# Kernel tuning notes

Hardware: AMD Instinct MI355X
Metric: run time of the kernel (lower is better)

## Reference

```python
import jax, jax.numpy as jnp
import numpy as np

B, N, DIM, EMB_H, EXP, K = 1, 1024, 64, 64, 4, 16


def setup_inputs() -> dict:
    key = jax.random.key(0)
    ks = jax.random.split(key, 12)
    s = lambda k, *shape: jax.random.normal(k, shape, dtype=jnp.float32) * 0.05
    return {
        "x": jax.random.normal(ks[0], (B, N, DIM), dtype=jnp.float32),
        "pos": jax.random.normal(ks[1], (B, N, 3), dtype=jnp.float32),
        "Wq": s(ks[2], DIM, DIM),
        "Wk": s(ks[3], DIM, DIM),
        "Wv": s(ks[4], DIM, DIM),
        "P1": s(ks[5], 3, EMB_H), "pb1": jnp.zeros((EMB_H,), jnp.float32),
        "P2": s(ks[6], EMB_H, DIM), "pb2": jnp.zeros((DIM,), jnp.float32),
        "A1": s(ks[7], DIM, DIM * EXP), "ab1": jnp.zeros((DIM * EXP,), jnp.float32),
        "A2": s(ks[8], DIM * EXP, DIM), "ab2": jnp.zeros((DIM,), jnp.float32),
        "nneighbors": K,
    }


def reference(x, pos, Wq, Wk, Wv, P1, pb1, P2, pb2, A1, ab1, A2, ab2, nneighbors):
    b, n, d = x.shape
    q = x @ Wq            # [b,n,d]
    k = x @ Wk
    v = x @ Wv
    qk_rel = q[:, :, None, :] - k[:, None, :, :]          # [b,n,n,d]
    rel_pos = pos[:, :, None, :] - pos[:, None, :, :]      # [b,n,n,3]
    rel_pos_emb = jax.nn.relu(rel_pos @ P1 + pb1) @ P2 + pb2  # [b,n,n,d]
    # kNN selection on euclidean distance (smallest nneighbors)
    rel_dist = jnp.linalg.norm(rel_pos, axis=-1)           # [b,n,n]
    _, idx = jax.lax.top_k(-rel_dist, nneighbors)          # [b,n,K]
    bidx = jnp.arange(b)[:, None, None]
    v_g = v[bidx, idx]                                     # [b,n,K,d]
    qk_g = jnp.take_along_axis(qk_rel, idx[..., None], axis=2)        # [b,n,K,d]
    rpe_g = jnp.take_along_axis(rel_pos_emb, idx[..., None], axis=2)  # [b,n,K,d]
    v_g = v_g + rpe_g
    sim = jax.nn.relu((qk_g + rpe_g) @ A1 + ab1) @ A2 + ab2  # [b,n,K,d]
    attn = jax.nn.softmax(sim, axis=-2)                      # softmax over neighbors
    agg = jnp.sum(attn * v_g, axis=2)                        # [b,n,d]
    return agg
```

## Files before the change

### kernel.cpp

```cpp
#include <hip/hip_runtime.h>

#define NPTS 1024
#define DIMD 64
#define KNN  16
#define HID  256
#define EMBH 64

typedef short short8 __attribute__((ext_vector_type(8)));
typedef float f32x4  __attribute__((ext_vector_type(4)));

__device__ __forceinline__ short f2bf(float x) {
    unsigned u = __float_as_uint(x);
    unsigned r = (u + 0x7fffu + ((u >> 16) & 1u)) >> 16;
    return (short)r;
}
__device__ __forceinline__ float bf2f(short s) {
    return __uint_as_float(((unsigned)(unsigned short)s) << 16);
}

#define AOFF(k, m) ((((k) >> 3) * 16 + (m)) * 8 + ((k) & 7))

__device__ __host__ __forceinline__ int frag_off(int K, int k, int n) {
    int T = n >> 4, c = k >> 5, q = (k >> 3) & 3, j = k & 7;
    int lane = (q << 4) | (n & 15);
    return ((T * (K >> 5) + c) * 64 + lane) * 8 + j;
}

#define A1HI 0
#define A1LO 16384
#define A2HI 32768
#define A2LO 49152
#define WKHI 65536
#define WKLO 69632
#define WVHI 73728
#define WVLO 77824
#define P2HI 81920
#define P2LO 86016

__global__ __launch_bounds__(256) void prep_weights(
    const float* __restrict__ A1, const float* __restrict__ A2,
    const float* __restrict__ Wk, const float* __restrict__ Wv,
    const float* __restrict__ P2, short* __restrict__ ws)
{
    int e = blockIdx.x * 256 + threadIdx.x;
    float v; int hi_base, lo_base, off;
    if (e < 16384)      { int k = e >> 8, n = e & 255;               v = A1[e];
                          hi_base = A1HI; lo_base = A1LO; off = frag_off(64,  k, n); }
    else if (e < 32768) { int t = e - 16384; int k = t >> 6, n = t & 63; v = A2[t];
                          hi_base = A2HI; lo_base = A2LO; off = frag_off(256, k, n); }
    else if (e < 36864) { int t = e - 32768; int k = t >> 6, n = t & 63; v = Wk[t];
                          hi_base = WKHI; lo_base = WKLO; off = frag_off(64,  k, n); }
    else if (e < 40960) { int t = e - 36864; int k = t >> 6, n = t & 63; v = Wv[t];
                          hi_base = WVHI; lo_base = WVLO; off = frag_off(64,  k, n); }
    else if (e < 45056) { int t = e - 40960; int k = t >> 6, n = t & 63; v = P2[t];
                          hi_base = P2HI; lo_base = P2LO; off = frag_off(64,  k, n); }
    else return;
    short h = f2bf(v);
    short l = f2bf(v - bf2f(h));
    ws[hi_base + off] = h;
    ws[lo_base + off] = l;
}

__global__ __launch_bounds__(256, 4) void ptl_fused(
    const float* __restrict__ x,  const float* __restrict__ pos,
    const float* __restrict__ Wq,
    const float* __restrict__ P1, const float* __restrict__ pb1,
    const float* __restrict__ pb2,
    const float* __restrict__ ab1, const float* __restrict__ ab2,
    const short* __restrict__ ws,
    float* __restrict__ out)
{
    __shared__ __align__(16) short a_xn_hi[16*64],  a_xn_lo[16*64];
    __shared__ __align__(16) short a_es_hi[16*64],  a_es_lo[16*64];
    __shared__ __align__(16) short a_h_hi [16*64],  a_h_lo [16*64];
    __shared__ __align__(16) short a_hd_hi[16*256], a_hd_lo[16*256];
    __shared__ __align__(16) float s_vg[16*68];
    __shared__ __align__(16) float s_sim[16*68];
    __shared__ float s_q[DIMD];
    __shared__ float s_cd[64];
    __shared__ int   s_ci[64];
    __shared__ int   s_idx[KNN];

    const int i    = blockIdx.x;
    const int tid  = threadIdx.x;
    const int lane = tid & 63;
    const int w    = tid >> 6;
    const int q4   = lane >> 4;
    const int col  = lane & 15;

    const float px = pos[i*3+0], py = pos[i*3+1], pz = pos[i*3+2];

    {
        const int base = w * 256;
        float du[4];
        #pragma unroll
        for (int u = 0; u < 4; u++) {
            int j = base + u * 64 + lane;
            float dx = __fsub_rn(px, pos[j*3+0]);
            float dy = __fsub_rn(py, pos[j*3+1]);
            float dz = __fsub_rn(pz, pos[j*3+2]);
            float s  = __fadd_rn(__fadd_rn(__fmul_rn(dx,dx), __fmul_rn(dy,dy)), __fmul_rn(dz,dz));
            du[u] = __fsqrt_rn(s);
        }
        for (int sel = 0; sel < KNN; sel++) {
            float mv = du[0]; int mu = 0;
            #pragma unroll
            for (int u = 1; u < 4; u++) if (du[u] < mv) { mv = du[u]; mu = u; }
            int mj = base + mu * 64 + lane;
            #pragma unroll
            for (int off = 32; off > 0; off >>= 1) {
                float ov = __shfl_xor(mv, off);
                int   oj = __shfl_xor(mj, off);
                if (ov < mv || (ov == mv && oj < mj)) { mv = ov; mj = oj; }
            }
            if (lane == 0) { s_cd[w * 16 + sel] = mv; s_ci[w * 16 + sel] = mj; }
            #pragma unroll
            for (int u = 0; u < 4; u++) if (base + u * 64 + lane == mj) du[u] = 3.0e38f;
        }
    }
    __syncthreads();

    if (w == 0) {
        float md = s_cd[lane]; int mi = s_ci[lane];
        for (int sel = 0; sel < KNN; sel++) {
            float mv = md; int mj = mi;
            #pragma unroll
            for (int off = 32; off > 0; off >>= 1) {
                float ov = __shfl_xor(mv, off);
                int   oj = __shfl_xor(mj, off);
                if (ov < mv || (ov == mv && oj < mj)) { mv = ov; mj = oj; }
            }
            if (lane == 0) s_idx[sel] = mj;
            if (mi == mj) md = 3.0e38f;
        }
    } else if (w == 1) {
        int d = lane;
        const float4* xr = (const float4*)(x + i * DIMD);
        float aq = 0.f;
        #pragma unroll
        for (int cb = 0; cb < DIMD / 4; cb++) {
            float4 xv = xr[cb];
            const float* wq = Wq + (cb*4) * DIMD + d;
            aq = fmaf(xv.x, wq[0*DIMD], aq); aq = fmaf(xv.y, wq[1*DIMD], aq);
            aq = fmaf(xv.z, wq[2*DIMD], aq); aq = fmaf(xv.w, wq[3*DIMD], aq);
        }
        s_q[d] = aq;
    }
    __syncthreads();

    #pragma unroll
    for (int u = 0; u < 4; u++) {
        int t = tid + 256 * u;
        int kk = t >> 6, c = t & 63;
        int j = s_idx[kk];
        int ao = AOFF(c, kk);
        float xv = x[j * DIMD + c];
        short xh = f2bf(xv);
        a_xn_hi[ao] = xh;
        a_xn_lo[ao] = f2bf(xv - bf2f(xh));
        float dx = px - pos[j*3+0];
        float dy = py - pos[j*3+1];
        float dz = pz - pos[j*3+2];
        float a = pb1[c];
        a = fmaf(dx, P1[0*EMBH+c], a);
        a = fmaf(dy, P1[1*EMBH+c], a);
        a = fmaf(dz, P1[2*EMBH+c], a);
        a = fmaxf(a, 0.0f);
        short eh = f2bf(a);
        a_es_hi[ao] = eh;
        a_es_lo[ao] = f2bf(a - bf2f(eh));
    }
    __syncthreads();

    const short8* wsv  = (const short8*)ws;
    const short8* xnh  = (const short8*)a_xn_hi;
    const short8* xnl  = (const short8*)a_xn_lo;
    const short8* esh  = (const short8*)a_es_hi;
    const short8* esl  = (const short8*)a_es_lo;
    const short8* hhv  = (const short8*)a_h_hi;
    const short8* hlv  = (const short8*)a_h_lo;
    const short8* hdh  = (const short8*)a_hd_hi;
    const short8* hdl  = (const short8*)a_hd_lo;

    auto bfrag = [&](int short_base, int f) -> short8 {
        return wsv[(short_base >> 3) + f * 64 + lane];
    };

    {
        f32x4 acck = {0,0,0,0}, accv = {0,0,0,0}, accr = {0,0,0,0};
        #pragma unroll
        for (int c = 0; c < 2; c++) {
            int av = (4*c + q4) * 16 + col;
            short8 xh = xnh[av], xl = xnl[av];
            int f = w * 2 + c;
            short8 bh = bfrag(WKHI, f), bl = bfrag(WKLO, f);
            acck = __builtin_amdgcn_mfma_f32_16x16x32_bf16(xh, bh, acck, 0,0,0);
            acck = __builtin_amdgcn_mfma_f32_16x16x32_bf16(xh, bl, acck, 0,0,0);
            acck = __builtin_amdgcn_mfma_f32_16x16x32_bf16(xl, bh, acck, 0,0,0);
        }
        #pragma unroll
        for (int c = 0; c < 2; c++) {
            int av = (4*c + q4) * 16 + col;
            short8 xh = xnh[av], xl = xnl[av];
            int f = w * 2 + c;
            short8 bh = bfrag(WVHI, f), bl = bfrag(WVLO, f);
            accv = __builtin_amdgcn_mfma_f32_16x16x32_bf16(xh, bh, accv, 0,0,0);
            accv = __builtin_amdgcn_mfma_f32_16x16x32_bf16(xh, bl, accv, 0,0,0);
            accv = __builtin_amdgcn_mfma_f32_16x16x32_bf16(xl, bh, accv, 0,0,0);
        }
        #pragma unroll
        for (int c = 0; c < 2; c++) {
            int av = (4*c + q4) * 16 + col;
            short8 eh = esh[av], el = esl[av];
            int f = w * 2 + c;
            short8 bh = bfrag(P2HI, f), bl = bfrag(P2LO, f);
            accr = __builtin_amdgcn_mfma_f32_16x16x32_bf16(eh, bh, accr, 0,0,0);
            accr = __builtin_amdgcn_mfma_f32_16x16x32_bf16(eh, bl, accr, 0,0,0);
            accr = __builtin_amdgcn_mfma_f32_16x16x32_bf16(el, bh, accr, 0,0,0);
        }
        int d = w * 16 + col;
        float qd = s_q[d], pb = pb2[d];
        #pragma unroll
        for (int r = 0; r < 4; r++) {
            int s = q4 * 4 + r;
            float rpe = accr[r] + pb;
            float hv  = qd - acck[r] + rpe;
            s_vg[s * 68 + d] = accv[r] + rpe;
            int ao = AOFF(d, s);
            short hh = f2bf(hv);
            a_h_hi[ao] = hh;
            a_h_lo[ao] = f2bf(hv - bf2f(hh));
        }
    }
    __syncthreads();

    {
        short8 hh[2], hl[2];
        #pragma unroll
        for (int c = 0; c < 2; c++) {
            int av = (4*c + q4) * 16 + col;
            hh[c] = hhv[av]; hl[c] = hlv[av];
        }
        #pragma unroll
        for (int t = 0; t < 4; t++) {
            int T = w * 4 + t;
            f32x4 acc = {0,0,0,0};
            #pragma unroll
            for (int c = 0; c < 2; c++) {
                int f = T * 2 + c;
                short8 bh = bfrag(A1HI, f), bl = bfrag(A1LO, f);
                acc = __builtin_amdgcn_mfma_f32_16x16x32_bf16(hh[c], bh, acc, 0,0,0);
                acc = __builtin_amdgcn_mfma_f32_16x16x32_bf16(hh[c], bl, acc, 0,0,0);
                acc = __builtin_amdgcn_mfma_f32_16x16x32_bf16(hl[c], bh, acc, 0,0,0);
            }
            int n = T * 16 + col;
            float bias = ab1[n];
            #pragma unroll
            for (int r = 0; r < 4; r++) {
                float val = fmaxf(acc[r] + bias, 0.0f);
                int ao = AOFF(n, q4 * 4 + r);
                short vh = f2bf(val);
                a_hd_hi[ao] = vh;
                a_hd_lo[ao] = f2bf(val - bf2f(vh));
            }
        }
    }
    __syncthreads();

    {
        f32x4 acc0 = {0,0,0,0}, acc1 = {0,0,0,0};
        #pragma unroll
        for (int c = 0; c < 8; c += 2) {
            {
                int av = (4*c + q4) * 16 + col;
                short8 ah = hdh[av], al = hdl[av];
                int f = w * 8 + c;
                short8 bh = bfrag(A2HI, f), bl = bfrag(A2LO, f);
                acc0 = __builtin_amdgcn_mfma_f32_16x16x32_bf16(ah, bh, acc0, 0,0,0);
                acc0 = __builtin_amdgcn_mfma_f32_16x16x32_bf16(ah, bl, acc0, 0,0,0);
                acc0 = __builtin_amdgcn_mfma_f32_16x16x32_bf16(al, bh, acc0, 0,0,0);
            }
            {
                int av = (4*(c+1) + q4) * 16 + col;
                short8 ah = hdh[av], al = hdl[av];
                int f = w * 8 + c + 1;
                short8 bh = bfrag(A2HI, f), bl = bfrag(A2LO, f);
                acc1 = __builtin_amdgcn_mfma_f32_16x16x32_bf16(ah, bh, acc1, 0,0,0);
                acc1 = __builtin_amdgcn_mfma_f32_16x16x32_bf16(ah, bl, acc1, 0,0,0);
                acc1 = __builtin_amdgcn_mfma_f32_16x16x32_bf16(al, bh, acc1, 0,0,0);
            }
        }
        int n = w * 16 + col;
        float bias = ab2[n];
        #pragma unroll
        for (int r = 0; r < 4; r++)
            s_sim[(q4 * 4 + r) * 68 + n] = acc0[r] + acc1[r] + bias;
    }
    __syncthreads();

    if (tid < DIMD) {
        int d = tid;
        float mx = -3.0e38f;
        #pragma unroll
        for (int kk = 0; kk < KNN; kk++) mx = fmaxf(mx, s_sim[kk * 68 + d]);
        float den = 0.0f, num = 0.0f;
        #pragma unroll
        for (int kk = 0; kk < KNN; kk++) {
            float e = expf(s_sim[kk * 68 + d] - mx);
            den += e;
            num = fmaf(e, s_vg[kk * 68 + d], num);
        }
        out[i * DIMD + d] = num / den;
    }
}

extern "C" void kernel_launch(void* const* d_in, const int* in_sizes, int n_in,
                              void* d_out, int out_size, void* d_ws, size_t ws_size,
                              hipStream_t stream) {
    const float* x   = (const float*)d_in[0];
    const float* pos = (const float*)d_in[1];
    const float* Wq  = (const float*)d_in[2];
    const float* Wk  = (const float*)d_in[3];
    const float* Wv  = (const float*)d_in[4];
    const float* P1  = (const float*)d_in[5];
    const float* pb1 = (const float*)d_in[6];
    const float* P2  = (const float*)d_in[7];
    const float* pb2 = (const float*)d_in[8];
    const float* A1  = (const float*)d_in[9];
    const float* ab1 = (const float*)d_in[10];
    const float* A2  = (const float*)d_in[11];
    const float* ab2 = (const float*)d_in[12];
    float* out = (float*)d_out;
    short* ws  = (short*)d_ws;

    prep_weights<<<(45056 + 255) / 256, 256, 0, stream>>>(A1, A2, Wk, Wv, P2, ws);
    ptl_fused<<<NPTS, 256, 0, stream>>>(x, pos, Wq, P1, pb1, pb2, ab1, ab2, ws, out);
}
```

Measured before the change: 110.4 us.

## Replace iterative kNN with radix select and drop weight low-bf16 split

```diff
diff --git a/kernel.cpp b/kernel.cpp
--- a/kernel.cpp
+++ b/kernel.cpp
@@ -1,4 +1,5 @@
 #include <hip/hip_runtime.h>
+#include <climits>
 
 #define NPTS 1024
 #define DIMD 64
@@ -26,16 +27,11 @@
     return ((T * (K >> 5) + c) * 64 + lane) * 8 + j;
 }
 
-#define A1HI 0
-#define A1LO 16384
-#define A2HI 32768
-#define A2LO 49152
-#define WKHI 65536
-#define WKLO 69632
-#define WVHI 73728
-#define WVLO 77824
-#define P2HI 81920
-#define P2LO 86016
+#define A1H 0
+#define A2H 16384
+#define WKH 32768
+#define WVH 36864
+#define P2H 40960
 
 __global__ __launch_bounds__(256) void prep_weights(
     const float* __restrict__ A1, const float* __restrict__ A2,
@@ -43,22 +39,19 @@
     const float* __restrict__ P2, short* __restrict__ ws)
 {
     int e = blockIdx.x * 256 + threadIdx.x;
-    float v; int hi_base, lo_base, off;
+    float v; int base, off;
     if (e < 16384)      { int k = e >> 8, n = e & 255;               v = A1[e];
-                          hi_base = A1HI; lo_base = A1LO; off = frag_off(64,  k, n); }
+                          base = A1H; off = frag_off(64,  k, n); }
     else if (e < 32768) { int t = e - 16384; int k = t >> 6, n = t & 63; v = A2[t];
-                          hi_base = A2HI; lo_base = A2LO; off = frag_off(256, k, n); }
+                          base = A2H; off = frag_off(256, k, n); }
     else if (e < 36864) { int t = e - 32768; int k = t >> 6, n = t & 63; v = Wk[t];
-                          hi_base = WKHI; lo_base = WKLO; off = frag_off(64,  k, n); }
+                          base = WKH; off = frag_off(64,  k, n); }
     else if (e < 40960) { int t = e - 36864; int k = t >> 6, n = t & 63; v = Wv[t];
-                          hi_base = WVHI; lo_base = WVLO; off = frag_off(64,  k, n); }
+                          base = WVH; off = frag_off(64,  k, n); }
     else if (e < 45056) { int t = e - 40960; int k = t >> 6, n = t & 63; v = P2[t];
-                          hi_base = P2HI; lo_base = P2LO; off = frag_off(64,  k, n); }
+                          base = P2H; off = frag_off(64,  k, n); }
     else return;
-    short h = f2bf(v);
-    short l = f2bf(v - bf2f(h));
-    ws[hi_base + off] = h;
-    ws[lo_base + off] = l;
+    ws[base + off] = f2bf(v);
 }
 
 __global__ __launch_bounds__(256, 4) void ptl_fused(
@@ -77,9 +70,9 @@
     __shared__ __align__(16) float s_vg[16*68];
     __shared__ __align__(16) float s_sim[16*68];
     __shared__ float s_q[DIMD];
-    __shared__ float s_cd[64];
-    __shared__ int   s_ci[64];
     __shared__ int   s_idx[KNN];
+    __shared__ int   s_cnt, s_cnt2, s_need;
+    __shared__ unsigned s_pref;
 
     const int i    = blockIdx.x;
     const int tid  = threadIdx.x;
@@ -90,48 +83,96 @@
 
     const float px = pos[i*3+0], py = pos[i*3+1], pz = pos[i*3+2];
 
-    {
-        const int base = w * 256;
-        float du[4];
+    unsigned ku[4];
+    #pragma unroll
+    for (int u = 0; u < 4; u++) {
+        int j = tid + 256 * u;
+        float dx = __fsub_rn(px, pos[j*3+0]);
+        float dy = __fsub_rn(py, pos[j*3+1]);
+        float dz = __fsub_rn(pz, pos[j*3+2]);
+        float s  = __fadd_rn(__fadd_rn(__fmul_rn(dx,dx), __fmul_rn(dy,dy)), __fmul_rn(dz,dz));
+        ku[u] = __float_as_uint(__fsqrt_rn(s));
+    }
+
+    int* histI = (int*)a_hd_hi;
+    int* s_tie = (int*)a_hd_lo;
+    if (tid == 0) { s_cnt = 0; s_cnt2 = 0; s_pref = 0u; s_need = KNN; }
+
+    for (int r = 0; r < 4; r++) {
+        const int shift = 24 - 8 * r;
+        for (int t = tid; t < 4 * 257; t += 256) histI[t] = 0;
+        __syncthreads();
+        unsigned pref = s_pref;
         #pragma unroll
         for (int u = 0; u < 4; u++) {
-            int j = base + u * 64 + lane;
-            float dx = __fsub_rn(px, pos[j*3+0]);
-            float dy = __fsub_rn(py, pos[j*3+1]);
-            float dz = __fsub_rn(pz, pos[j*3+2]);
-            float s  = __fadd_rn(__fadd_rn(__fmul_rn(dx,dx), __fmul_rn(dy,dy)), __fmul_rn(dz,dz));
-            du[u] = __fsqrt_rn(s);
-        }
-        for (int sel = 0; sel < KNN; sel++) {
-            float mv = du[0]; int mu = 0;
-            #pragma unroll
-            for (int u = 1; u < 4; u++) if (du[u] < mv) { mv = du[u]; mu = u; }
-            int mj = base + mu * 64 + lane;
-            #pragma unroll
-            for (int off = 32; off > 0; off >>= 1) {
-                float ov = __shfl_xor(mv, off);
-                int   oj = __shfl_xor(mj, off);
-                if (ov < mv || (ov == mv && oj < mj)) { mv = ov; mj = oj; }
-            }
-            if (lane == 0) { s_cd[w * 16 + sel] = mv; s_ci[w * 16 + sel] = mj; }
-            #pragma unroll
-            for (int u = 0; u < 4; u++) if (base + u * 64 + lane == mj) du[u] = 3.0e38f;
-        }
+            unsigned k = ku[u];
+            bool match = true;
+            if (r > 0) match = ((k >> (shift + 8)) == (pref >> (shift + 8)));
+            if (match) atomicAdd(&histI[w * 257 + ((k >> shift) & 255)], 1);
+        }
+        __syncthreads();
+        if (w == 0) {
+            int b0 = lane * 4, cnt4[4], loc = 0;
+            #pragma unroll
+            for (int t = 0; t < 4; t++) {
+                int s = 0;
+                #pragma unroll
+                for (int ww = 0; ww < 4; ww++) s += histI[ww * 257 + b0 + t];
+                cnt4[t] = s; loc += s;
+            }
+            int incl = loc;
+            #pragma unroll
+            for (int off = 1; off < 64; off <<= 1) {
+                int t = __shfl_up(incl, off);
+                if (lane >= off) incl += t;
+            }
+            int excl = incl - loc;
+            int need = s_need;
+            unsigned long long mk = __ballot(incl >= need);
+            int lstar = (int)__ffsll((long long)mk) - 1;
+            if (lane == lstar) {
+                int run = excl, t = 0;
+                while (t < 3 && run + cnt4[t] < need) { run += cnt4[t]; t++; }
+                s_pref = pref | ((unsigned)(b0 + t) << shift);
+                s_need = need - run;
+            }
+        }
+        __syncthreads();
+    }
+    const unsigned T = s_pref;
+    const int needT  = s_need;
+
+    #pragma unroll
+    for (int u = 0; u < 4; u++) {
+        unsigned k = ku[u];
+        int j = tid + 256 * u;
+        if (k < T)       { int p = atomicAdd(&s_cnt, 1);  s_idx[p] = j; }
+        else if (k == T) { int p = atomicAdd(&s_cnt2, 1); if (p < 256) s_tie[p] = j; }
     }
     __syncthreads();
 
     if (w == 0) {
-        float md = s_cd[lane]; int mi = s_ci[lane];
-        for (int sel = 0; sel < KNN; sel++) {
-            float mv = md; int mj = mi;
-            #pragma unroll
-            for (int off = 32; off > 0; off >>= 1) {
-                float ov = __shfl_xor(mv, off);
-                int   oj = __shfl_xor(mj, off);
-                if (ov < mv || (ov == mv && oj < mj)) { mv = ov; mj = oj; }
-            }
-            if (lane == 0) s_idx[sel] = mj;
-            if (mi == mj) md = 3.0e38f;
+        int base = s_cnt;
+        int m = s_cnt2;
+        if (m == needT) {
+            for (int t = lane; t < m; t += 64) s_idx[base + t] = s_tie[t];
+        } else {
+            int cand[4];
+            #pragma unroll
+            for (int t = 0; t < 4; t++) {
+                int e = lane + 64 * t;
+                cand[t] = (e < m && e < 256) ? s_tie[e] : INT_MAX;
+            }
+            for (int sel = 0; sel < needT; sel++) {
+                int mv = cand[0];
+                #pragma unroll
+                for (int t = 1; t < 4; t++) mv = min(mv, cand[t]);
+                #pragma unroll
+                for (int off = 32; off > 0; off >>= 1) mv = min(mv, __shfl_xor(mv, off));
+                #pragma unroll
+                for (int t = 0; t < 4; t++) if (cand[t] == mv) cand[t] = INT_MAX;
+                if (lane == 0) s_idx[base + sel] = mv;
+            }
         }
     } else if (w == 1) {
         int d = lane;
@@ -193,30 +234,20 @@
             int av = (4*c + q4) * 16 + col;
             short8 xh = xnh[av], xl = xnl[av];
             int f = w * 2 + c;
-            short8 bh = bfrag(WKHI, f), bl = bfrag(WKLO, f);
-            acck = __builtin_amdgcn_mfma_f32_16x16x32_bf16(xh, bh, acck, 0,0,0);
-            acck = __builtin_amdgcn_mfma_f32_16x16x32_bf16(xh, bl, acck, 0,0,0);
-            acck = __builtin_amdgcn_mfma_f32_16x16x32_bf16(xl, bh, acck, 0,0,0);
-        }
-        #pragma unroll
-        for (int c = 0; c < 2; c++) {
-            int av = (4*c + q4) * 16 + col;
-            short8 xh = xnh[av], xl = xnl[av];
-            int f = w * 2 + c;
-            short8 bh = bfrag(WVHI, f), bl = bfrag(WVLO, f);
-            accv = __builtin_amdgcn_mfma_f32_16x16x32_bf16(xh, bh, accv, 0,0,0);
-            accv = __builtin_amdgcn_mfma_f32_16x16x32_bf16(xh, bl, accv, 0,0,0);
-            accv = __builtin_amdgcn_mfma_f32_16x16x32_bf16(xl, bh, accv, 0,0,0);
+            short8 bk = bfrag(WKH, f);
+            short8 bv = bfrag(WVH, f);
+            acck = __builtin_amdgcn_mfma_f32_16x16x32_bf16(xh, bk, acck, 0,0,0);
+            acck = __builtin_amdgcn_mfma_f32_16x16x32_bf16(xl, bk, acck, 0,0,0);
+            accv = __builtin_amdgcn_mfma_f32_16x16x32_bf16(xh, bv, accv, 0,0,0);
+            accv = __builtin_amdgcn_mfma_f32_16x16x32_bf16(xl, bv, accv, 0,0,0);
         }
         #pragma unroll
         for (int c = 0; c < 2; c++) {
             int av = (4*c + q4) * 16 + col;
             short8 eh = esh[av], el = esl[av];
-            int f = w * 2 + c;
-            short8 bh = bfrag(P2HI, f), bl = bfrag(P2LO, f);
-            accr = __builtin_amdgcn_mfma_f32_16x16x32_bf16(eh, bh, accr, 0,0,0);
-            accr = __builtin_amdgcn_mfma_f32_16x16x32_bf16(eh, bl, accr, 0,0,0);
-            accr = __builtin_amdgcn_mfma_f32_16x16x32_bf16(el, bh, accr, 0,0,0);
+            short8 bp = bfrag(P2H, w * 2 + c);
+            accr = __builtin_amdgcn_mfma_f32_16x16x32_bf16(eh, bp, accr, 0,0,0);
+            accr = __builtin_amdgcn_mfma_f32_16x16x32_bf16(el, bp, accr, 0,0,0);
         }
         int d = w * 16 + col;
         float qd = s_q[d], pb = pb2[d];
@@ -243,17 +274,15 @@
         }
         #pragma unroll
         for (int t = 0; t < 4; t++) {
-            int T = w * 4 + t;
+            int T4 = w * 4 + t;
             f32x4 acc = {0,0,0,0};
             #pragma unroll
             for (int c = 0; c < 2; c++) {
-                int f = T * 2 + c;
-                short8 bh = bfrag(A1HI, f), bl = bfrag(A1LO, f);
+                short8 bh = bfrag(A1H, T4 * 2 + c);
                 acc = __builtin_amdgcn_mfma_f32_16x16x32_bf16(hh[c], bh, acc, 0,0,0);
-                acc = __builtin_amdgcn_mfma_f32_16x16x32_bf16(hh[c], bl, acc, 0,0,0);
                 acc = __builtin_amdgcn_mfma_f32_16x16x32_bf16(hl[c], bh, acc, 0,0,0);
             }
-            int n = T * 16 + col;
+            int n = T4 * 16 + col;
             float bias = ab1[n];
             #pragma unroll
             for (int r = 0; r < 4; r++) {
@@ -274,19 +303,15 @@
             {
                 int av = (4*c + q4) * 16 + col;
                 short8 ah = hdh[av], al = hdl[av];
-                int f = w * 8 + c;
-                short8 bh = bfrag(A2HI, f), bl = bfrag(A2LO, f);
+                short8 bh = bfrag(A2H, w * 8 + c);
                 acc0 = __builtin_amdgcn_mfma_f32_16x16x32_bf16(ah, bh, acc0, 0,0,0);
-                acc0 = __builtin_amdgcn_mfma_f32_16x16x32_bf16(ah, bl, acc0, 0,0,0);
                 acc0 = __builtin_amdgcn_mfma_f32_16x16x32_bf16(al, bh, acc0, 0,0,0);
             }
             {
                 int av = (4*(c+1) + q4) * 16 + col;
                 short8 ah = hdh[av], al = hdl[av];
-                int f = w * 8 + c + 1;
-                short8 bh = bfrag(A2HI, f), bl = bfrag(A2LO, f);
+                short8 bh = bfrag(A2H, w * 8 + c + 1);
                 acc1 = __builtin_amdgcn_mfma_f32_16x16x32_bf16(ah, bh, acc1, 0,0,0);
-                acc1 = __builtin_amdgcn_mfma_f32_16x16x32_bf16(ah, bl, acc1, 0,0,0);
                 acc1 = __builtin_amdgcn_mfma_f32_16x16x32_bf16(al, bh, acc1, 0,0,0);
             }
         }
```

After: 95.97 us. 1.15x faster.
